# Optimization experiments

Hardware: AMD Instinct MI355X
Metric: run time of the kernel (lower is better)

Reference implementation:

```python
import jax, jax.numpy as jnp
import numpy as np

B, N, DIM = 32, 3136, 64
H, DH, AGENTS = 8, 8, 49
INNER = H * DH  # 64
SCALE = DH ** -0.5


def setup_inputs() -> dict:
    key = jax.random.key(0)
    ks = jax.random.split(key, 7)
    s = 0.05
    return {
        "x1": jax.random.normal(ks[0], (B, N, DIM), jnp.float32),
        "x2": jax.random.normal(ks[1], (B, N, INNER), jnp.float32),
        "Wq": jax.random.normal(ks[2], (INNER, DIM), jnp.float32) * s,   # to_q (out,in)
        "Wk": jax.random.normal(ks[3], (DIM, INNER), jnp.float32) * s,   # to_k
        "Wv": jax.random.normal(ks[4], (DIM, INNER), jnp.float32) * s,   # to_v
        "Wo": jax.random.normal(ks[5], (2 * DIM, 2 * DIM), jnp.float32) * s,  # to_out linear
        "bo": jax.random.normal(ks[6], (2 * DIM,), jnp.float32) * s,
    }


def _split_heads(t):
    # (b, n, h*d) -> (b, h, n, d)
    b, n, hd = t.shape
    return t.reshape(b, n, H, hd // H).transpose(0, 2, 1, 3)


def reference(x1, x2, Wq, Wk, Wv, Wo, bo):
    b, n, _ = x1.shape
    q = x1 @ Wq.T                      # (b, n, 64)
    k = x2 @ Wk.T                      # (b, n, dim=64)
    v = x2 @ Wv.T
    # AdaptiveAvgPool2d((49, dim)): n % 49 == 0 and channel 64->64 is identity,
    # so pooling is an exact block mean over the sequence axis.
    agent = q.reshape(b, AGENTS, n // AGENTS, q.shape[-1]).mean(axis=2)  # (b, 49, 64)

    agent_h = _split_heads(agent)      # (b, h, 49, d)
    q1 = _split_heads(q)               # (b, h, n, d)
    k_h = _split_heads(k)
    v_h = _split_heads(v)

    # stage 0: agent tokens attend over keys/values (dropout is identity at eval)
    dots0 = jnp.einsum('bhid,bhjd->bhij', agent_h, k_h) * SCALE   # (b,h,49,n)
    attn0 = jax.nn.softmax(dots0, axis=-1)
    out0 = jnp.einsum('bhij,bhjd->bhid', attn0, v_h)              # (b,h,49,d)

    # stage 1: queries attend over agent tokens
    dots1 = jnp.einsum('bhid,bhjd->bhij', q1, agent_h) * SCALE    # (b,h,n,49)
    attn1 = jax.nn.softmax(dots1, axis=-1)
    out1 = jnp.einsum('bhij,bhjd->bhid', attn1, out0)             # (b,h,n,d)

    out1 = out1.transpose(0, 2, 1, 3).reshape(b, n, -1)           # (b,n,64)
    out1 = jnp.concatenate([out1, x1], axis=-1)                   # (b,n,128)
    return out1 @ Wo.T + bo
```

## Files before the change

### kernel.cpp

```cpp
#include <hip/hip_runtime.h>
#include <hip/hip_bf16.h>

#define NB 32
#define NSEQ 3136
#define NDIM 64
#define NH 8
#define NAG 49
#define NPAIR 25

static constexpr float kScale = 0.35355339059327378f;
static constexpr float kLog2e = 1.4426950408889634f;

typedef unsigned short us;
typedef __attribute__((ext_vector_type(8))) __bf16 bf16x8;
typedef __attribute__((ext_vector_type(4))) __bf16 bf16x4;
typedef __attribute__((ext_vector_type(2))) _Float16 f16x2;
typedef __attribute__((ext_vector_type(4))) _Float16 f16x4;
typedef __attribute__((ext_vector_type(8))) _Float16 f16x8;
typedef __attribute__((ext_vector_type(4))) float f32x4;

__device__ __forceinline__ float fexp2(float x) {
#if __has_builtin(__builtin_amdgcn_exp2f)
  return __builtin_amdgcn_exp2f(x);
#else
  return exp2f(x);
#endif
}

__device__ __forceinline__ float frcp(float x) {
#if __has_builtin(__builtin_amdgcn_rcpf)
  return __builtin_amdgcn_rcpf(x);
#else
  return 1.f / x;
#endif
}

__device__ __forceinline__ unsigned pk2(float a, float b) {
#if __has_builtin(__builtin_amdgcn_cvt_pkrtz)
  return __builtin_bit_cast(unsigned, __builtin_amdgcn_cvt_pkrtz(a, b));
#else
  f16x2 v = {(_Float16)a, (_Float16)b};
  return __builtin_bit_cast(unsigned, v);
#endif
}

__device__ __forceinline__ bf16x8 ldw8(const float* W, int row, int c0, int ld) {
  const float4* p = (const float4*)(W + (size_t)row * ld + c0);
  float4 v0 = p[0], v1 = p[1];
  bf16x8 r;
  r[0]=(__bf16)v0.x; r[1]=(__bf16)v0.y; r[2]=(__bf16)v0.z; r[3]=(__bf16)v0.w;
  r[4]=(__bf16)v1.x; r[5]=(__bf16)v1.y; r[6]=(__bf16)v1.z; r[7]=(__bf16)v1.w;
  return r;
}

__global__ __launch_bounds__(256) void agent_x1_kernel(
    const float* __restrict__ x1, const float* __restrict__ Wq,
    us* __restrict__ x1bf, us* __restrict__ agf16) {
  __shared__ float red[4][64];
  __shared__ float marr[64];
  const int a = blockIdx.x, b = blockIdx.y, t = threadIdx.x;
  const int i64 = t & 63, cb = t >> 6;

  {
    const float4* s1 = (const float4*)(x1 + ((size_t)(b * NSEQ) + a * 64 + i64) * NDIM + cb * 16);
    float4 v0 = s1[0], v1 = s1[1], v2 = s1[2], v3 = s1[3];
    bf16x8 p0, p1;
    p0[0]=(__bf16)v0.x; p0[1]=(__bf16)v0.y; p0[2]=(__bf16)v0.z; p0[3]=(__bf16)v0.w;
    p0[4]=(__bf16)v1.x; p0[5]=(__bf16)v1.y; p0[6]=(__bf16)v1.z; p0[7]=(__bf16)v1.w;
    p1[0]=(__bf16)v2.x; p1[1]=(__bf16)v2.y; p1[2]=(__bf16)v2.z; p1[3]=(__bf16)v2.w;
    p1[4]=(__bf16)v3.x; p1[5]=(__bf16)v3.y; p1[6]=(__bf16)v3.z; p1[7]=(__bf16)v3.w;
    __bf16* dst = (__bf16*)x1bf;
    *(bf16x8*)(dst + ((((size_t)b * NAG + a) * 8 + cb * 2) * 64 + i64) * 8) = p0;
    *(bf16x8*)(dst + ((((size_t)b * NAG + a) * 8 + cb * 2 + 1) * 64 + i64) * 8) = p1;
  }
  {
    const float* xc = x1 + ((size_t)(b * NSEQ) + a * 64 + cb * 16) * NDIM + i64;
    float cs = 0.f;
#pragma unroll
    for (int i = 0; i < 16; ++i) cs += xc[i * NDIM];
    red[cb][i64] = cs;
  }
  __syncthreads();
  if (t < 64) marr[t] = red[0][t] + red[1][t] + red[2][t] + red[3][t];
  __syncthreads();
  if (t < 64) {
    const float4* wqr = (const float4*)(Wq + (size_t)t * NDIM);
    const float4* mm = (const float4*)marr;
    float s0 = 0.f;
#pragma unroll
    for (int i = 0; i < 16; ++i) {
      float4 wv4 = wqr[i], m4 = mm[i];
      s0 += wv4.x * m4.x + wv4.y * m4.y + wv4.z * m4.z + wv4.w * m4.w;
    }
    const float val = s0 * (kScale * kLog2e / 64.f);
    ((_Float16*)agf16)[(((size_t)b * NH + (t >> 3)) * NAG + a) * 8 + (t & 7)] =
        (_Float16)val;
  }
}

__global__ __launch_bounds__(256) void kv_stage0_kernel(
    const float* __restrict__ x2, const float* __restrict__ Wk,
    const float* __restrict__ Wv, const us* __restrict__ agf16,
    us* __restrict__ pvp) {
  __shared__ __align__(16) __bf16 xb[64][72];
  __shared__ __align__(16) _Float16 klds[4][64][24];
  __shared__ __align__(16) _Float16 vlds[4][18][72];
  __shared__ __align__(16) _Float16 plds[4][64][40];
  const int pair = blockIdx.x, b = blockIdx.y, t = threadIdx.x;
  const int i64 = t & 63, cb = t >> 6;
  const int w = cb, lr = (t >> 4) & 3, lc = t & 15;

  bf16x8 ak0 = ldw8(Wk, w * 16 + lc, lr * 8, NDIM);
  bf16x8 ak1 = ldw8(Wk, w * 16 + lc, 32 + lr * 8, NDIM);
  bf16x8 av0 = ldw8(Wv, w * 16 + lc, lr * 8, NDIM);
  bf16x8 av1 = ldw8(Wv, w * 16 + lc, 32 + lr * 8, NDIM);

  const size_t bh0 = (size_t)b * NH + 2 * w;
  f16x8 ba[2][4];
#pragma unroll
  for (int hh = 0; hh < 2; ++hh)
#pragma unroll
    for (int at = 0; at < 4; ++at) {
      f16x8 v = (f16x8)(_Float16)0.0f;
      if (lr == 0) {
        int row = at * 16 + lc; if (row > 48) row = 48;
        v = *(const f16x8*)(agf16 + (bh0 + hh) * (NAG * 8) + row * 8);
      }
      ba[hh][at] = v;
    }
  vlds[w][16][i64] = (_Float16)1.0f;

  f32x4 accPV[2][4];
#pragma unroll
  for (int hh = 0; hh < 2; ++hh)
#pragma unroll
    for (int i = 0; i < 4; ++i) accPV[hh][i] = (f32x4){0.f, 0.f, 0.f, 0.f};

  for (int cc = 0; cc < 2; ++cc) {
    const int a = pair * 2 + cc;
    if (a >= NAG) break;
    if (cc) __syncthreads();

    {
      const float4* s2 = (const float4*)(x2 + ((size_t)(b * NSEQ) + a * 64 + i64) * NDIM + cb * 16);
      float4 v0 = s2[0], v1 = s2[1], v2 = s2[2], v3 = s2[3];
      bf16x8 p0, p1;
      p0[0]=(__bf16)v0.x; p0[1]=(__bf16)v0.y; p0[2]=(__bf16)v0.z; p0[3]=(__bf16)v0.w;
      p0[4]=(__bf16)v1.x; p0[5]=(__bf16)v1.y; p0[6]=(__bf16)v1.z; p0[7]=(__bf16)v1.w;
      p1[0]=(__bf16)v2.x; p1[1]=(__bf16)v2.y; p1[2]=(__bf16)v2.z; p1[3]=(__bf16)v2.w;
      p1[4]=(__bf16)v3.x; p1[5]=(__bf16)v3.y; p1[6]=(__bf16)v3.z; p1[7]=(__bf16)v3.w;
      *(bf16x8*)&xb[i64][cb * 16] = p0; *(bf16x8*)&xb[i64][cb * 16 + 8] = p1;
    }
    __syncthreads();

    f32x4 acck[4], accv[4];
#pragma unroll
    for (int i = 0; i < 4; ++i) {
      acck[i] = (f32x4){0.f, 0.f, 0.f, 0.f};
      accv[i] = (f32x4){0.f, 0.f, 0.f, 0.f};
    }
#pragma unroll
    for (int nt = 0; nt < 4; ++nt) {
      bf16x8 x0 = *(const bf16x8*)&xb[nt * 16 + lc][lr * 8];
      bf16x8 x1f = *(const bf16x8*)&xb[nt * 16 + lc][32 + lr * 8];
      acck[nt] = __builtin_amdgcn_mfma_f32_16x16x32_bf16(ak0, x0, acck[nt], 0, 0, 0);
      acck[nt] = __builtin_amdgcn_mfma_f32_16x16x32_bf16(ak1, x1f, acck[nt], 0, 0, 0);
      accv[nt] = __builtin_amdgcn_mfma_f32_16x16x32_bf16(av0, x0, accv[nt], 0, 0, 0);
      accv[nt] = __builtin_amdgcn_mfma_f32_16x16x32_bf16(av1, x1f, accv[nt], 0, 0, 0);
    }
#pragma unroll
    for (int nt = 0; nt < 4; ++nt) {
      f16x4 pk4;
      pk4[0]=(_Float16)acck[nt][0]; pk4[1]=(_Float16)acck[nt][1];
      pk4[2]=(_Float16)acck[nt][2]; pk4[3]=(_Float16)acck[nt][3];
      *(f16x4*)&klds[w][nt * 16 + lc][lr * 4] = pk4;
#pragma unroll
      for (int j = 0; j < 4; ++j)
        vlds[w][lr * 4 + j][nt * 16 + lc] = (_Float16)accv[nt][j];
    }

#pragma unroll
    for (int hh = 0; hh < 2; ++hh) {
#pragma unroll
      for (int half = 0; half < 2; ++half) {
#pragma unroll
        for (int tb = 0; tb < 2; ++tb) {
          const int tokbase = half * 32 + tb * 16;
          f16x8 kf = *(const f16x8*)&klds[w][tokbase + lc][hh * 8];
#pragma unroll
          for (int at = 0; at < 4; ++at) {
            f32x4 sc = __builtin_amdgcn_mfma_f32_16x16x32_f16(
                kf, ba[hh][at], (f32x4){0.f, 0.f, 0.f, 0.f}, 0, 0, 0);
            unsigned u0 = pk2(fexp2(sc[0]), fexp2(sc[1]));
            unsigned u1 = pk2(fexp2(sc[2]), fexp2(sc[3]));
            unsigned long long q = ((unsigned long long)u1 << 32) | u0;
            *(unsigned long long*)&plds[w][at * 16 + lc][tb * 16 + lr * 4] = q;
          }
        }
        const int frow = (lc < 8) ? hh * 8 + lc : 16;
        f16x8 vf = *(const f16x8*)&vlds[w][frow][half * 32 + lr * 8];
#pragma unroll
        for (int at = 0; at < 4; ++at) {
          f16x8 pf = *(const f16x8*)&plds[w][at * 16 + lc][lr * 8];
          accPV[hh][at] =
              __builtin_amdgcn_mfma_f32_16x16x32_f16(pf, vf, accPV[hh][at], 0, 0, 0);
        }
      }
    }
  }

#pragma unroll
  for (int hh = 0; hh < 2; ++hh) {
    if (lc < 9) {
      _Float16* dst = (_Float16*)pvp + ((bh0 + hh) * NPAIR + pair) * 441;
#pragma unroll
      for (int at = 0; at < 4; ++at)
#pragma unroll
        for (int j = 0; j < 4; ++j) {
          const int ag = at * 16 + lr * 4 + j;
          if (ag < NAG) dst[ag * 9 + lc] = (_Float16)accPV[hh][at][j];
        }
    }
  }
}

__global__ __launch_bounds__(256) void aofin_kernel(
    const us* __restrict__ pvp, us* __restrict__ pvtF) {
  __shared__ float acc[441];
  const int h = blockIdx.x, b = blockIdx.y, t = threadIdx.x;
  const size_t bh = (size_t)b * NH + h;
  const _Float16* src = (const _Float16*)pvp + bh * (NPAIR * 441);
  for (int s = t; s < 441; s += 256) {
    float v = 0.f;
#pragma unroll 5
    for (int p = 0; p < NPAIR; ++p) v += (float)src[(size_t)p * 441 + s];
    acc[s] = v;
  }
  __syncthreads();
  if (t < 64) {
    us* col = pvtF + bh * 1024 + t;
    float inv = (t < NAG) ? frcp(acc[t * 9 + 8]) : 0.f;
#pragma unroll
    for (int f = 0; f < 8; ++f) {
      float val = (t < NAG) ? acc[t * 9 + f] * inv : 0.f;
      _Float16 hv = (_Float16)val;
      col[f * 64] = __builtin_bit_cast(us, hv);
    }
    col[8 * 64] = (t < NAG) ? (us)0x3C00 : (us)0;
#pragma unroll
    for (int f = 9; f < 16; ++f) col[f * 64] = 0;
  }
}

__global__ __launch_bounds__(512, 8) void stage1_out_kernel(
    const us* __restrict__ x1bf, const float* __restrict__ Wq,
    const us* __restrict__ agf16, const us* __restrict__ pvtF,
    const float* __restrict__ Wo, const float* __restrict__ bo,
    float* __restrict__ out) {
  __shared__ __align__(16) __bf16 xa[64][72];
  __shared__ __align__(16) us qcat[64][72];
  __shared__ __align__(16) _Float16 pW[8][16][72];
  const int tile = blockIdx.x, b = blockIdx.y;
  const int t = threadIdx.x, tokl = t & 63, h = t >> 6;
  const int w = h, lane = t & 63, lr = (lane >> 4) & 3, lc = lane & 15;
  const int mtile = w & 3, thalf = w >> 2;
  const size_t bh = (size_t)b * NH + w;

  bf16x8 wqf0 = ldw8(Wq, mtile * 16 + lc, lr * 8, NDIM);
  bf16x8 wqf1 = ldw8(Wq, mtile * 16 + lc, 32 + lr * 8, NDIM);

  f16x8 ba[4];
#pragma unroll
  for (int at = 0; at < 4; ++at) {
    f16x8 v = (f16x8)(_Float16)0.0f;
    if (lr == 0) {
      int row = at * 16 + lc; if (row > 48) row = 48;
      v = *(const f16x8*)(agf16 + bh * (NAG * 8) + row * 8);
    }
    ba[at] = v;
  }
  const us* pvb = pvtF + bh * 1024;
  f16x8 pvB0 = *(const f16x8*)(pvb + lc * 64 + lr * 8);
  f16x8 pvB1 = *(const f16x8*)(pvb + lc * 64 + 32 + lr * 8);

  {
    bf16x8 p = *(const bf16x8*)((const __bf16*)x1bf +
        ((((size_t)b * NAG + tile) * 8 + h) * 64 + tokl) * 8);
    *(bf16x8*)&xa[tokl][h * 8] = p;
  }
  __syncthreads();

  {
    f32x4 aq[2];
    aq[0] = (f32x4){0.f,0.f,0.f,0.f}; aq[1] = (f32x4){0.f,0.f,0.f,0.f};
#pragma unroll
    for (int nt = 0; nt < 2; ++nt) {
      bf16x8 bx0 = *(const bf16x8*)&xa[thalf * 32 + nt * 16 + lc][lr * 8];
      bf16x8 bx1 = *(const bf16x8*)&xa[thalf * 32 + nt * 16 + lc][32 + lr * 8];
      aq[nt] = __builtin_amdgcn_mfma_f32_16x16x32_bf16(wqf0, bx0, aq[nt], 0, 0, 0);
      aq[nt] = __builtin_amdgcn_mfma_f32_16x16x32_bf16(wqf1, bx1, aq[nt], 0, 0, 0);
    }
#pragma unroll
    for (int nt = 0; nt < 2; ++nt) {
      f16x4 pk;
      pk[0]=(_Float16)aq[nt][0]; pk[1]=(_Float16)aq[nt][1];
      pk[2]=(_Float16)aq[nt][2]; pk[3]=(_Float16)aq[nt][3];
      *(f16x4*)&qcat[thalf * 32 + nt * 16 + lc][mtile * 16 + lr * 4] = pk;
    }
  }
  __syncthreads();

  {
    _Float16* psw = &pW[w][0][0];
#pragma unroll 1
    for (int g = 0; g < 4; ++g) {
      f16x8 qf = *(const f16x8*)&qcat[g * 16 + lc][w * 8];
#pragma unroll
      for (int at = 0; at < 4; ++at) {
        f32x4 sc = __builtin_amdgcn_mfma_f32_16x16x32_f16(
            ba[at], qf, (f32x4){0.f, 0.f, 0.f, 0.f}, 0, 0, 0);
        unsigned u0 = pk2(fexp2(sc[0]), fexp2(sc[1]));
        unsigned u1 = pk2(fexp2(sc[2]), fexp2(sc[3]));
        unsigned long long qq = ((unsigned long long)u1 << 32) | u0;
        *(unsigned long long*)&psw[(size_t)lc * 72 + at * 16 + lr * 4] = qq;
      }
      f16x8 pA0 = *(const f16x8*)&psw[(size_t)lc * 72 + lr * 8];
      f16x8 pA1 = *(const f16x8*)&psw[(size_t)lc * 72 + 32 + lr * 8];
      f32x4 pv = __builtin_amdgcn_mfma_f32_16x16x32_f16(
          pvB0, pA0, (f32x4){0.f, 0.f, 0.f, 0.f}, 0, 0, 0);
      pv = __builtin_amdgcn_mfma_f32_16x16x32_f16(pvB1, pA1, pv, 0, 0, 0);
      float den = __shfl(pv[0], 32 + lc);
      float inv = frcp(den);
      if (lr < 2) {
        bf16x4 pc;
        pc[0] = (__bf16)(pv[0] * inv); pc[1] = (__bf16)(pv[1] * inv);
        pc[2] = (__bf16)(pv[2] * inv); pc[3] = (__bf16)(pv[3] * inv);
        *(bf16x4*)((__bf16*)&qcat[g * 16 + lc][0] + w * 8 + lr * 4) = pc;
      }
    }
  }
  bf16x8 wof[4];
#pragma unroll
  for (int ks = 0; ks < 4; ++ks)
    wof[ks] = ldw8(Wo, w * 16 + lc, ks * 32 + lr * 8, 128);
  f32x4 bv = *(const f32x4*)(bo + w * 16 + lr * 4);
  __syncthreads();

  {
    f32x4 acc[4];
#pragma unroll
    for (int i = 0; i < 4; ++i) acc[i] = (f32x4){0.f,0.f,0.f,0.f};
#pragma unroll
    for (int ks = 0; ks < 4; ++ks) {
#pragma unroll
      for (int nt = 0; nt < 4; ++nt) {
        bf16x8 bx = (ks < 2) ? *(const bf16x8*)&qcat[nt * 16 + lc][ks * 32 + lr * 8]
                             : *(const bf16x8*)&xa[nt * 16 + lc][(ks - 2) * 32 + lr * 8];
        acc[nt] = __builtin_amdgcn_mfma_f32_16x16x32_bf16(wof[ks], bx, acc[nt], 0, 0, 0);
      }
    }
#pragma unroll
    for (int nt = 0; nt < 4; ++nt) {
      f32x4 v = acc[nt] + bv;
      float* dst = out + ((size_t)b * NSEQ + tile * 64 + nt * 16 + lc) * 128 + w * 16 + lr * 4;
      *(f32x4*)dst = v;
    }
  }
}

extern "C" void kernel_launch(void* const* d_in, const int* in_sizes, int n_in,
                              void* d_out, int out_size, void* d_ws, size_t ws_size,
                              hipStream_t stream) {
  (void)in_sizes; (void)n_in; (void)out_size; (void)ws_size;
  const float* x1 = (const float*)d_in[0];
  const float* x2 = (const float*)d_in[1];
  const float* Wq = (const float*)d_in[2];
  const float* Wk = (const float*)d_in[3];
  const float* Wv = (const float*)d_in[4];
  const float* Wo = (const float*)d_in[5];
  const float* bo = (const float*)d_in[6];
  float* out = (float*)d_out;

  us* x1bf = (us*)d_ws;
  us* agf16 = x1bf + (size_t)NB * NSEQ * 64;
  us* pvp = agf16 + (size_t)NB * NH * NAG * 8;
  us* pvtF = pvp + (size_t)NB * NH * NPAIR * 441;

  agent_x1_kernel<<<dim3(NAG, NB), 256, 0, stream>>>(x1, Wq, x1bf, agf16);
  kv_stage0_kernel<<<dim3(NPAIR, NB), 256, 0, stream>>>(x2, Wk, Wv, agf16, pvp);
  aofin_kernel<<<dim3(NH, NB), 256, 0, stream>>>(pvp, pvtF);
  stage1_out_kernel<<<dim3(NAG, NB), 512, 0, stream>>>(x1bf, Wq, agf16,
                                                       pvtF, Wo, bo, out);
}
```

Baseline: 76.37 us.

## Fuse stage0 reduction into kv kernel via last-block ticket, split output GEMM

```diff
diff --git a/kernel.cpp b/kernel.cpp
--- a/kernel.cpp
+++ b/kernel.cpp
@@ -55,11 +55,13 @@
 
 __global__ __launch_bounds__(256) void agent_x1_kernel(
     const float* __restrict__ x1, const float* __restrict__ Wq,
-    us* __restrict__ x1bf, us* __restrict__ agf16) {
+    us* __restrict__ x1bf, us* __restrict__ agf16, unsigned* __restrict__ ticket) {
   __shared__ float red[4][64];
   __shared__ float marr[64];
   const int a = blockIdx.x, b = blockIdx.y, t = threadIdx.x;
   const int i64 = t & 63, cb = t >> 6;
+
+  if (a == 0 && t == 0) ticket[b] = 0u;
 
   {
     const float4* s1 = (const float4*)(x1 + ((size_t)(b * NSEQ) + a * 64 + i64) * NDIM + cb * 16);
@@ -101,11 +103,12 @@
 __global__ __launch_bounds__(256) void kv_stage0_kernel(
     const float* __restrict__ x2, const float* __restrict__ Wk,
     const float* __restrict__ Wv, const us* __restrict__ agf16,
-    us* __restrict__ pvp) {
+    us* __restrict__ pvp, us* __restrict__ pvtF, unsigned* __restrict__ ticket) {
   __shared__ __align__(16) __bf16 xb[64][72];
   __shared__ __align__(16) _Float16 klds[4][64][24];
   __shared__ __align__(16) _Float16 vlds[4][18][72];
   __shared__ __align__(16) _Float16 plds[4][64][40];
+  __shared__ bool lastdone;
   const int pair = blockIdx.x, b = blockIdx.y, t = threadIdx.x;
   const int i64 = t & 63, cb = t >> 6;
   const int w = cb, lr = (t >> 4) & 3, lc = t & 15;
@@ -222,33 +225,37 @@
         }
     }
   }
-}
-
-__global__ __launch_bounds__(256) void aofin_kernel(
-    const us* __restrict__ pvp, us* __restrict__ pvtF) {
-  __shared__ float acc[441];
-  const int h = blockIdx.x, b = blockIdx.y, t = threadIdx.x;
-  const size_t bh = (size_t)b * NH + h;
-  const _Float16* src = (const _Float16*)pvp + bh * (NPAIR * 441);
-  for (int s = t; s < 441; s += 256) {
+
+  __threadfence();
+  __syncthreads();
+  if (t == 0) {
+    unsigned prev = atomicAdd(&ticket[b], 1u);
+    lastdone = (prev == NPAIR - 1);
+  }
+  __syncthreads();
+  if (!lastdone) return;
+  __threadfence();
+  float* accS = (float*)&plds[0][0][0];
+  for (int i = t; i < NH * 441; i += 256) {
+    const int hh = i / 441, s = i - hh * 441;
+    const _Float16* src = (const _Float16*)pvp +
+        (((size_t)b * NH + hh) * NPAIR) * 441 + s;
     float v = 0.f;
 #pragma unroll 5
-    for (int p = 0; p < NPAIR; ++p) v += (float)src[(size_t)p * 441 + s];
-    acc[s] = v;
-  }
-  __syncthreads();
-  if (t < 64) {
-    us* col = pvtF + bh * 1024 + t;
-    float inv = (t < NAG) ? frcp(acc[t * 9 + 8]) : 0.f;
-#pragma unroll
-    for (int f = 0; f < 8; ++f) {
-      float val = (t < NAG) ? acc[t * 9 + f] * inv : 0.f;
-      _Float16 hv = (_Float16)val;
-      col[f * 64] = __builtin_bit_cast(us, hv);
-    }
-    col[8 * 64] = (t < NAG) ? (us)0x3C00 : (us)0;
-#pragma unroll
-    for (int f = 9; f < 16; ++f) col[f * 64] = 0;
+    for (int p = 0; p < NPAIR; ++p) v += (float)src[(size_t)p * 441];
+    accS[i] = v;
+  }
+  __syncthreads();
+  for (int i = t; i < NH * 1024; i += 256) {
+    const int hh = i >> 10, rem = i & 1023, f = rem >> 6, ag = rem & 63;
+    float val = 0.f;
+    if (ag < NAG) {
+      const float* ah = accS + hh * 441;
+      if (f < 8) val = ah[ag * 9 + f] * frcp(ah[ag * 9 + 8]);
+      else if (f == 8) val = 1.f;
+    }
+    _Float16 hv = (_Float16)val;
+    pvtF[((size_t)b * NH + hh) * 1024 + f * 64 + ag] = __builtin_bit_cast(us, hv);
   }
 }
 
@@ -339,32 +346,33 @@
       }
     }
   }
-  bf16x8 wof[4];
-#pragma unroll
-  for (int ks = 0; ks < 4; ++ks)
-    wof[ks] = ldw8(Wo, w * 16 + lc, ks * 32 + lr * 8, 128);
+
+  bf16x8 wof0 = ldw8(Wo, w * 16 + lc, lr * 8, 128);
+  bf16x8 wof1 = ldw8(Wo, w * 16 + lc, 32 + lr * 8, 128);
+  bf16x8 wof2 = ldw8(Wo, w * 16 + lc, 64 + lr * 8, 128);
+  bf16x8 wof3 = ldw8(Wo, w * 16 + lc, 96 + lr * 8, 128);
   f32x4 bv = *(const f32x4*)(bo + w * 16 + lr * 4);
-  __syncthreads();
-
-  {
-    f32x4 acc[4];
-#pragma unroll
-    for (int i = 0; i < 4; ++i) acc[i] = (f32x4){0.f,0.f,0.f,0.f};
-#pragma unroll
-    for (int ks = 0; ks < 4; ++ks) {
-#pragma unroll
-      for (int nt = 0; nt < 4; ++nt) {
-        bf16x8 bx = (ks < 2) ? *(const bf16x8*)&qcat[nt * 16 + lc][ks * 32 + lr * 8]
-                             : *(const bf16x8*)&xa[nt * 16 + lc][(ks - 2) * 32 + lr * 8];
-        acc[nt] = __builtin_amdgcn_mfma_f32_16x16x32_bf16(wof[ks], bx, acc[nt], 0, 0, 0);
-      }
-    }
-#pragma unroll
-    for (int nt = 0; nt < 4; ++nt) {
-      f32x4 v = acc[nt] + bv;
-      float* dst = out + ((size_t)b * NSEQ + tile * 64 + nt * 16 + lc) * 128 + w * 16 + lr * 4;
-      *(f32x4*)dst = v;
-    }
+  f32x4 acc[4];
+#pragma unroll
+  for (int i = 0; i < 4; ++i) acc[i] = (f32x4){0.f,0.f,0.f,0.f};
+#pragma unroll
+  for (int nt = 0; nt < 4; ++nt) {
+    bf16x8 b0 = *(const bf16x8*)&xa[nt * 16 + lc][lr * 8];
+    bf16x8 b1 = *(const bf16x8*)&xa[nt * 16 + lc][32 + lr * 8];
+    acc[nt] = __builtin_amdgcn_mfma_f32_16x16x32_bf16(wof2, b0, acc[nt], 0, 0, 0);
+    acc[nt] = __builtin_amdgcn_mfma_f32_16x16x32_bf16(wof3, b1, acc[nt], 0, 0, 0);
+  }
+  __syncthreads();
+
+#pragma unroll
+  for (int nt = 0; nt < 4; ++nt) {
+    bf16x8 c0 = *(const bf16x8*)&qcat[nt * 16 + lc][lr * 8];
+    bf16x8 c1 = *(const bf16x8*)&qcat[nt * 16 + lc][32 + lr * 8];
+    acc[nt] = __builtin_amdgcn_mfma_f32_16x16x32_bf16(wof0, c0, acc[nt], 0, 0, 0);
+    acc[nt] = __builtin_amdgcn_mfma_f32_16x16x32_bf16(wof1, c1, acc[nt], 0, 0, 0);
+    f32x4 v = acc[nt] + bv;
+    float* dst = out + ((size_t)b * NSEQ + tile * 64 + nt * 16 + lc) * 128 + w * 16 + lr * 4;
+    *(f32x4*)dst = v;
   }
 }
 
@@ -385,10 +393,11 @@
   us* agf16 = x1bf + (size_t)NB * NSEQ * 64;
   us* pvp = agf16 + (size_t)NB * NH * NAG * 8;
   us* pvtF = pvp + (size_t)NB * NH * NPAIR * 441;
-
-  agent_x1_kernel<<<dim3(NAG, NB), 256, 0, stream>>>(x1, Wq, x1bf, agf16);
-  kv_stage0_kernel<<<dim3(NPAIR, NB), 256, 0, stream>>>(x2, Wk, Wv, agf16, pvp);
-  aofin_kernel<<<dim3(NH, NB), 256, 0, stream>>>(pvp, pvtF);
+  unsigned* ticket = (unsigned*)(pvtF + (size_t)NB * NH * 1024);
+
+  agent_x1_kernel<<<dim3(NAG, NB), 256, 0, stream>>>(x1, Wq, x1bf, agf16, ticket);
+  kv_stage0_kernel<<<dim3(NPAIR, NB), 256, 0, stream>>>(x2, Wk, Wv, agf16, pvp,
+                                                        pvtF, ticket);
   stage1_out_kernel<<<dim3(NAG, NB), 512, 0, stream>>>(x1bf, Wq, agf16,
                                                        pvtF, Wo, bo, out);
 }
```

Result: slower. 201.7 us (+164.1%).
